# Kernel optimization log

Measured on AMD Instinct MI355X. Metric: run time of the kernel, lower is better.

Reference implementation:

```python
import jax, jax.numpy as jnp
import numpy as np

H = 50  # hidden_size

def setup_inputs() -> dict:
    key = jax.random.key(0)
    ks = jax.random.split(key, 7)
    B, T = 2048, 1024
    s = 1.0 / np.sqrt(H)  # PyTorch default init scale
    return {
        "x": jax.random.normal(ks[0], (B, T, 1), dtype=jnp.float32),
        "W_ih": jax.random.uniform(ks[1], (4 * H, 1), jnp.float32, -s, s),
        "W_hh": jax.random.uniform(ks[2], (4 * H, H), jnp.float32, -s, s),
        "b_ih": jax.random.uniform(ks[3], (4 * H,), jnp.float32, -s, s),
        "b_hh": jax.random.uniform(ks[4], (4 * H,), jnp.float32, -s, s),
        "W_lin": jax.random.uniform(ks[5], (1, H), jnp.float32, -s, s),
        "b_lin": jax.random.uniform(ks[6], (1,), jnp.float32, -s, s),
    }

def reference(x, W_ih, W_hh, b_ih, b_hh, W_lin, b_lin):
    B, T, _ = x.shape
    # Precompute input contribution to gates for all timesteps: [T, B, 4H]
    gx = jnp.einsum('bti,gi->tbg', x, W_ih) + (b_ih + b_hh)

    def step(carry, gx_t):
        h, c = carry
        gates = gx_t + h @ W_hh.T               # [B, 4H]
        i, f, g, o = jnp.split(gates, 4, axis=-1)  # PyTorch gate order i,f,g,o
        i = jax.nn.sigmoid(i)
        f = jax.nn.sigmoid(f)
        g = jnp.tanh(g)
        o = jax.nn.sigmoid(o)
        c = f * c + i * g
        h = o * jnp.tanh(c)
        return (h, c), None

    h0 = jnp.zeros((B, H), x.dtype)
    c0 = jnp.zeros((B, H), x.dtype)
    (h_last, _), _ = jax.lax.scan(step, (h0, c0), gx)
    # Linear head on last timestep's hidden state -> [B, 1]
    return h_last @ W_lin.T + b_lin
```

## Files before the change

kernel.cpp:

```cpp
#include <hip/hip_runtime.h>


#define H     50
#define TT    1024
#define BATCH 2048
#define BW    8
#define NTHR  448
#define KP    72
#define KX_HI 50
#define KX_LO 51
#define KX_H2 52
#define KB_HI 53
#define KB_LO 54

typedef float    f32x4 __attribute__((ext_vector_type(4)));
typedef _Float16 f16x8 __attribute__((ext_vector_type(8)));

__global__ __launch_bounds__(NTHR, 1) void lstm_kernel(
    const float* __restrict__ x,
    const float* __restrict__ W_ih,
    const float* __restrict__ W_hh,
    const float* __restrict__ b_ih,
    const float* __restrict__ b_hh,
    const float* __restrict__ W_lin,
    const float* __restrict__ b_lin,
    float* __restrict__ out)
{
    __shared__ _Float16 hb[2][16][KP];
    __shared__ float    redH[H][BW];

    const int tid  = threadIdx.x;
    const int wave = tid >> 6;
    const int lane = tid & 63;
    const int L15  = lane & 15;
    const int kq   = lane >> 4;
    const int bl   = L15 & 7;
    const int b0   = blockIdx.x * BW;

    const int t0 = 2 * wave;

    const float LOG2E  = 1.4426950408889634f;
    const float LOG2E2 = 2.8853900817779268f;

    f16x8 A[2][2];
    #pragma unroll
    for (int tt = 0; tt < 2; ++tt) {
        const int m  = (t0 + tt) * 16 + L15;
        const int jm = m >> 2, gm = m & 3;
        const float s = (gm == 2) ? LOG2E2 : -LOG2E;
        float swih = 0.f, sbias = 0.f;
        if (jm < H) {
            swih  = s * W_ih[gm * H + jm];
            sbias = s * (b_ih[gm * H + jm] + b_hh[gm * H + jm]);
        }
        const _Float16 whi = (_Float16)swih;
        const _Float16 wlo = (_Float16)(swih - (float)whi);
        const _Float16 bhi = (_Float16)sbias;
        const _Float16 blo = (_Float16)(sbias - (float)bhi);
        #pragma unroll
        for (int kf = 0; kf < 2; ++kf) {
            f16x8 v;
            #pragma unroll
            for (int e = 0; e < 8; ++e) {
                const int k = kf * 32 + kq * 8 + e;
                _Float16 val = (_Float16)0.f;
                if (jm < H) {
                    if (k < H)            val = (_Float16)(s * W_hh[(gm * H + jm) * H + k]);
                    else if (k == KX_HI)  val = whi;
                    else if (k == KX_LO)  val = whi;
                    else if (k == KX_H2)  val = wlo;
                    else if (k == KB_HI)  val = bhi;
                    else if (k == KB_LO)  val = blo;
                }
                v[e] = val;
            }
            A[tt][kf] = v;
        }
    }

    const int  j  = 4 * t0 + kq + ((L15 >> 3) << 2);
    const bool jv = (j < H);
    const float wlin = jv ? W_lin[j] : 0.f;

    for (int i = tid; i < 2 * 16 * KP; i += NTHR)
        ((_Float16*)hb)[i] = (_Float16)0.f;
    __syncthreads();
    if (tid < 32) {
        hb[tid >> 4][tid & 15][KB_HI] = (_Float16)1.0f;
        hb[tid >> 4][tid & 15][KB_LO] = (_Float16)1.0f;
    } else if (tid < 48) {
        const int col = tid & 15;
        const float xv = x[(size_t)(b0 + (col & 7)) * TT];
        const _Float16 xh = (_Float16)xv;
        hb[0][col][KX_HI] = xh;
        hb[0][col][KX_LO] = (_Float16)(xv - (float)xh);
        hb[0][col][KX_H2] = xh;
    }

    const float* xrow = x + (size_t)(b0 + bl) * TT;
    float4 xq = {0,0,0,0}, xq2 = {0,0,0,0};
    if (wave == 0) {
        xq  = *(const float4*)(xrow);
        xq2 = *(const float4*)(xrow + 4);
    }

    float c = 0.f, hlast = 0.f;
    __syncthreads();

    for (int t = 0; t < TT; ++t) {
        const _Float16* hp = &hb[t & 1][L15][0];
        f16x8 B0 = *(const f16x8*)(hp + kq * 8);
        f16x8 B1 = *(const f16x8*)(hp + 32 + kq * 8);

        f32x4 z = {0.f, 0.f, 0.f, 0.f};
        f32x4 a0 = __builtin_amdgcn_mfma_f32_16x16x32_f16(A[0][0], B0, z, 0, 0, 0);
        f32x4 a1 = __builtin_amdgcn_mfma_f32_16x16x32_f16(A[1][0], B0, z, 0, 0, 0);
        a0 = __builtin_amdgcn_mfma_f32_16x16x32_f16(A[0][1], B1, a0, 0, 0, 0);
        a1 = __builtin_amdgcn_mfma_f32_16x16x32_f16(A[1][1], B1, a1, 0, 0, 0);

        const int idx = t + 1;
        const int nb  = idx & 1;

        if (wave == 0) {
            if ((idx & 3) == 0) {
                xq = xq2;
                int o = idx + 4; if (o > TT - 4) o = TT - 4;
                xq2 = *(const float4*)(xrow + o);
            }
            const float xv = ((const float*)&xq)[idx & 3];
            if (kq < 3) {
                const _Float16 xh = (_Float16)xv;
                const _Float16 xl = (_Float16)(xv - (float)xh);
                const int slot = (kq == 0) ? KX_HI : (kq == 1) ? KX_LO : KX_H2;
                hb[nb][L15][slot] = (kq == 1) ? xl : xh;
            }
        }

        const bool lo = (L15 < 8);
        const float zi = lo ? a0[0] : a1[0];
        const float zf = lo ? a0[1] : a1[1];
        const float zg = lo ? a0[2] : a1[2];
        const float zo = lo ? a0[3] : a1[3];
        const float i_ = __builtin_amdgcn_rcpf(1.0f + __builtin_amdgcn_exp2f(zi));
        const float f_ = __builtin_amdgcn_rcpf(1.0f + __builtin_amdgcn_exp2f(zf));
        const float o_ = __builtin_amdgcn_rcpf(1.0f + __builtin_amdgcn_exp2f(zo));
        const float g_ = __builtin_fmaf(-2.0f,
            __builtin_amdgcn_rcpf(1.0f + __builtin_amdgcn_exp2f(zg)), 1.0f);
        c = __builtin_fmaf(f_, c, i_ * g_);
        const float tc_ = __builtin_fmaf(-2.0f,
            __builtin_amdgcn_rcpf(1.0f + __builtin_amdgcn_exp2f(LOG2E2 * c)), 1.0f);
        const float h = o_ * tc_;
        hlast = h;

        if (jv) {
            const _Float16 hh = (_Float16)h;
            hb[nb][bl][j]     = hh;
            hb[nb][bl + 8][j] = hh;
        }
        __syncthreads();
    }

    if (jv) redH[j][bl] = wlin * hlast;
    __syncthreads();
    if (tid < BW) {
        float s = b_lin[0];
        #pragma unroll 10
        for (int jj = 0; jj < H; ++jj) s += redH[jj][tid];
        out[b0 + tid] = s;
    }
}

extern "C" void kernel_launch(void* const* d_in, const int* in_sizes, int n_in,
                              void* d_out, int out_size, void* d_ws, size_t ws_size,
                              hipStream_t stream) {
    const float* x     = (const float*)d_in[0];
    const float* W_ih  = (const float*)d_in[1];
    const float* W_hh  = (const float*)d_in[2];
    const float* b_ih  = (const float*)d_in[3];
    const float* b_hh  = (const float*)d_in[4];
    const float* W_lin = (const float*)d_in[5];
    const float* b_lin = (const float*)d_in[6];
    float* out = (float*)d_out;

    dim3 grid(BATCH / BW);
    dim3 block(NTHR);
    lstm_kernel<<<grid, block, 0, stream>>>(x, W_ih, W_hh, b_ih, b_hh,
                                            W_lin, b_lin, out);
}
```

Baseline: 389.2 us.

## Shrink LSTM block to 4 batch rows and 4 waves, two blocks per CU

Each workgroup now handles 4 batch elements with 4 waves instead of 8 elements with 7 waves. Each wave issues up to 8 MFMAs per step covering 4 gate tiles, and wave 3 does only 2. The B operand lanes duplicate 4 batch columns instead of 8, and launch bounds allow 2 blocks per CU. This doubles the number of workgroups so more CUs and occupancy are used. In exchange, each wave does more MFMA work per step and a larger share of each 16-column MFMA is redundant.

Result: slower. 489.4 us (+25.8%).

```diff
diff --git a/kernel.cpp b/kernel.cpp
--- a/kernel.cpp
+++ b/kernel.cpp
@@ -4,9 +4,9 @@
 #define H     50
 #define TT    1024
 #define BATCH 2048
-#define BW    8
-#define NTHR  448
-#define KP    72
+#define BW    4
+#define NTHR  256
+#define KP    80
 #define KX_HI 50
 #define KX_LO 51
 #define KX_H2 52
@@ -16,7 +16,7 @@
 typedef float    f32x4 __attribute__((ext_vector_type(4)));
 typedef _Float16 f16x8 __attribute__((ext_vector_type(8)));
 
-__global__ __launch_bounds__(NTHR, 1) void lstm_kernel(
+__global__ __launch_bounds__(NTHR, 2) void lstm_kernel(
     const float* __restrict__ x,
     const float* __restrict__ W_ih,
     const float* __restrict__ W_hh,
@@ -26,7 +26,7 @@
     const float* __restrict__ b_lin,
     float* __restrict__ out)
 {
-    __shared__ _Float16 hb[2][16][KP];
+    __shared__ _Float16 hb[2][BW][KP];
     __shared__ float    redH[H][BW];
 
     const int tid  = threadIdx.x;
@@ -34,22 +34,23 @@
     const int lane = tid & 63;
     const int L15  = lane & 15;
     const int kq   = lane >> 4;
-    const int bl   = L15 & 7;
+    const int bl   = L15 & 3;
+    const int cp   = L15 >> 2;
     const int b0   = blockIdx.x * BW;
-
-    const int t0 = 2 * wave;
 
     const float LOG2E  = 1.4426950408889634f;
     const float LOG2E2 = 2.8853900817779268f;
 
-    f16x8 A[2][2];
+    f16x8 A[4][2];
     #pragma unroll
-    for (int tt = 0; tt < 2; ++tt) {
-        const int m  = (t0 + tt) * 16 + L15;
+    for (int i = 0; i < 4; ++i) {
+        const int T  = 4 * wave + i;
+        const int m  = T * 16 + L15;
         const int jm = m >> 2, gm = m & 3;
+        const bool v = (jm < H);
         const float s = (gm == 2) ? LOG2E2 : -LOG2E;
         float swih = 0.f, sbias = 0.f;
-        if (jm < H) {
+        if (v) {
             swih  = s * W_ih[gm * H + jm];
             sbias = s * (b_ih[gm * H + jm] + b_hh[gm * H + jm]);
         }
@@ -59,12 +60,12 @@
         const _Float16 blo = (_Float16)(sbias - (float)bhi);
         #pragma unroll
         for (int kf = 0; kf < 2; ++kf) {
-            f16x8 v;
+            f16x8 vv;
             #pragma unroll
             for (int e = 0; e < 8; ++e) {
                 const int k = kf * 32 + kq * 8 + e;
                 _Float16 val = (_Float16)0.f;
-                if (jm < H) {
+                if (v) {
                     if (k < H)            val = (_Float16)(s * W_hh[(gm * H + jm) * H + k]);
                     else if (k == KX_HI)  val = whi;
                     else if (k == KX_LO)  val = whi;
@@ -72,29 +73,29 @@
                     else if (k == KB_HI)  val = bhi;
                     else if (k == KB_LO)  val = blo;
                 }
-                v[e] = val;
+                vv[e] = val;
             }
-            A[tt][kf] = v;
+            A[i][kf] = vv;
         }
     }
 
-    const int  j  = 4 * t0 + kq + ((L15 >> 3) << 2);
+    const int  j  = 16 * wave + 4 * cp + kq;
     const bool jv = (j < H);
     const float wlin = jv ? W_lin[j] : 0.f;
 
-    for (int i = tid; i < 2 * 16 * KP; i += NTHR)
+    for (int i = tid; i < 2 * BW * KP; i += NTHR)
         ((_Float16*)hb)[i] = (_Float16)0.f;
     __syncthreads();
-    if (tid < 32) {
-        hb[tid >> 4][tid & 15][KB_HI] = (_Float16)1.0f;
-        hb[tid >> 4][tid & 15][KB_LO] = (_Float16)1.0f;
-    } else if (tid < 48) {
-        const int col = tid & 15;
-        const float xv = x[(size_t)(b0 + (col & 7)) * TT];
+    if (tid < 8) {
+        hb[tid >> 2][tid & 3][KB_HI] = (_Float16)1.0f;
+        hb[tid >> 2][tid & 3][KB_LO] = (_Float16)1.0f;
+    } else if (tid < 12) {
+        const int bb = tid - 8;
+        const float xv = x[(size_t)(b0 + bb) * TT];
         const _Float16 xh = (_Float16)xv;
-        hb[0][col][KX_HI] = xh;
-        hb[0][col][KX_LO] = (_Float16)(xv - (float)xh);
-        hb[0][col][KX_H2] = xh;
+        hb[0][bb][KX_HI] = xh;
+        hb[0][bb][KX_LO] = (_Float16)(xv - (float)xh);
+        hb[0][bb][KX_H2] = xh;
     }
 
     const float* xrow = x + (size_t)(b0 + bl) * TT;
@@ -108,15 +109,22 @@
     __syncthreads();
 
     for (int t = 0; t < TT; ++t) {
-        const _Float16* hp = &hb[t & 1][L15][0];
+        const _Float16* hp = &hb[t & 1][bl][0];
         f16x8 B0 = *(const f16x8*)(hp + kq * 8);
         f16x8 B1 = *(const f16x8*)(hp + 32 + kq * 8);
 
-        f32x4 z = {0.f, 0.f, 0.f, 0.f};
-        f32x4 a0 = __builtin_amdgcn_mfma_f32_16x16x32_f16(A[0][0], B0, z, 0, 0, 0);
-        f32x4 a1 = __builtin_amdgcn_mfma_f32_16x16x32_f16(A[1][0], B0, z, 0, 0, 0);
+        const f32x4 z = {0.f, 0.f, 0.f, 0.f};
+        f32x4 a0, a1 = z, a2 = z, a3 = z;
+        a0 = __builtin_amdgcn_mfma_f32_16x16x32_f16(A[0][0], B0, z, 0, 0, 0);
         a0 = __builtin_amdgcn_mfma_f32_16x16x32_f16(A[0][1], B1, a0, 0, 0, 0);
-        a1 = __builtin_amdgcn_mfma_f32_16x16x32_f16(A[1][1], B1, a1, 0, 0, 0);
+        if (wave != 3) {
+            a1 = __builtin_amdgcn_mfma_f32_16x16x32_f16(A[1][0], B0, z, 0, 0, 0);
+            a2 = __builtin_amdgcn_mfma_f32_16x16x32_f16(A[2][0], B0, z, 0, 0, 0);
+            a3 = __builtin_amdgcn_mfma_f32_16x16x32_f16(A[3][0], B0, z, 0, 0, 0);
+            a1 = __builtin_amdgcn_mfma_f32_16x16x32_f16(A[1][1], B1, a1, 0, 0, 0);
+            a2 = __builtin_amdgcn_mfma_f32_16x16x32_f16(A[2][1], B1, a2, 0, 0, 0);
+            a3 = __builtin_amdgcn_mfma_f32_16x16x32_f16(A[3][1], B1, a3, 0, 0, 0);
+        }
 
         const int idx = t + 1;
         const int nb  = idx & 1;
@@ -127,8 +135,8 @@
                 int o = idx + 4; if (o > TT - 4) o = TT - 4;
                 xq2 = *(const float4*)(xrow + o);
             }
-            const float xv = ((const float*)&xq)[idx & 3];
-            if (kq < 3) {
+            if (L15 < 4 && kq < 3) {
+                const float xv = ((const float*)&xq)[idx & 3];
                 const _Float16 xh = (_Float16)xv;
                 const _Float16 xl = (_Float16)(xv - (float)xh);
                 const int slot = (kq == 0) ? KX_HI : (kq == 1) ? KX_LO : KX_H2;
@@ -136,27 +144,22 @@
             }
         }
 
-        const bool lo = (L15 < 8);
-        const float zi = lo ? a0[0] : a1[0];
-        const float zf = lo ? a0[1] : a1[1];
-        const float zg = lo ? a0[2] : a1[2];
-        const float zo = lo ? a0[3] : a1[3];
-        const float i_ = __builtin_amdgcn_rcpf(1.0f + __builtin_amdgcn_exp2f(zi));
-        const float f_ = __builtin_amdgcn_rcpf(1.0f + __builtin_amdgcn_exp2f(zf));
-        const float o_ = __builtin_amdgcn_rcpf(1.0f + __builtin_amdgcn_exp2f(zo));
+        const f32x4 lo_  = (cp == 0) ? a0 : a1;
+        const f32x4 hi_  = (cp == 2) ? a2 : a3;
+        const f32x4 g4   = (cp < 2) ? lo_ : hi_;
+
+        const float i_ = __builtin_amdgcn_rcpf(1.0f + __builtin_amdgcn_exp2f(g4[0]));
+        const float f_ = __builtin_amdgcn_rcpf(1.0f + __builtin_amdgcn_exp2f(g4[1]));
         const float g_ = __builtin_fmaf(-2.0f,
-            __builtin_amdgcn_rcpf(1.0f + __builtin_amdgcn_exp2f(zg)), 1.0f);
+            __builtin_amdgcn_rcpf(1.0f + __builtin_amdgcn_exp2f(g4[2])), 1.0f);
+        const float o_ = __builtin_amdgcn_rcpf(1.0f + __builtin_amdgcn_exp2f(g4[3]));
         c = __builtin_fmaf(f_, c, i_ * g_);
         const float tc_ = __builtin_fmaf(-2.0f,
             __builtin_amdgcn_rcpf(1.0f + __builtin_amdgcn_exp2f(LOG2E2 * c)), 1.0f);
         const float h = o_ * tc_;
         hlast = h;
 
-        if (jv) {
-            const _Float16 hh = (_Float16)h;
-            hb[nb][bl][j]     = hh;
-            hb[nb][bl + 8][j] = hh;
-        }
+        if (jv) hb[nb][bl][j] = (_Float16)h;
         __syncthreads();
     }
 
```
